# Performance work log

Measured on AMD Instinct MI355X. Metric: run time of the kernel, lower is better.

## Reference

```python
import jax, jax.numpy as jnp
import numpy as np

# dimensions (match init_kwargs / input_specs)
K = 25        # number of observation events
N_PER = 2048  # observations per event
B = 4096      # batch (sample_idx length)
D = 64        # input_dim
NDIM = 8      # memory_dim
H = D * NDIM  # hidden = 512
STEPS = 2     # euler ODE steps between consecutive obs_times
DT = 0.01
LOG_SQRT_2PI = 0.9189385332046727  # log(sqrt(2*pi))


def _xavier(key, shape):
    lim = np.sqrt(6.0 / (shape[0] + shape[1])).astype(np.float32)
    return jax.random.uniform(key, shape, jnp.float32, -lim, lim)


def setup_inputs() -> dict:
    key = jax.random.key(0)
    ks = jax.random.split(key, 10)
    # unique per-event indices (matches torch scatter-assign semantics)
    rng = np.random.RandomState(0)
    batch_idx = jnp.asarray(
        np.stack([rng.permutation(B)[:N_PER] for _ in range(K)]).reshape(-1),
        jnp.int32)
    return {
        "obs_times": jnp.arange(1, K + 1, dtype=jnp.float32) * (STEPS * DT),
        "event_pt": jnp.arange(K + 1, dtype=jnp.int32) * N_PER,
        "sample_idx": jnp.arange(B, dtype=jnp.int32),
        "X": jax.random.normal(ks[0], (K * N_PER, D), jnp.float32),
        "M": (jax.random.uniform(ks[1], (K * N_PER, D)) < 0.8).astype(jnp.float32),
        "batch_idx": batch_idx,
        # ODEFunc: Linear(H,H) -> Tanh -> Linear(H,H)
        "W_ode1": _xavier(ks[2], (H, H)), "b_ode1": jnp.zeros((H,), jnp.float32),
        "W_ode2": _xavier(ks[3], (H, H)), "b_ode2": jnp.zeros((H,), jnp.float32),
        # GRUCell(D, H)
        "W_ih": _xavier(ks[4], (3 * H, D)), "W_hh": _xavier(ks[5], (3 * H, H)),
        "b_ih": jnp.zeros((3 * H,), jnp.float32), "b_hh": jnp.zeros((3 * H,), jnp.float32),
        # p_model: Linear(H,H) -> ReLU -> (dropout=0) -> Linear(H, 2D)
        "Wp1": _xavier(ks[6], (H, H)), "bp1": jnp.zeros((H,), jnp.float32),
        "Wp2": _xavier(ks[7], (2 * D, H)), "bp2": jnp.zeros((2 * D,), jnp.float32),
    }


def reference(obs_times, event_pt, sample_idx, X, M, batch_idx,
              W_ode1, b_ode1, W_ode2, b_ode2,
              W_ih, W_hh, b_ih, b_hh, Wp1, bp1, Wp2, bp2):
    Xr = X.reshape(K, N_PER, D)
    Mr = M.reshape(K, N_PER, D)
    idx = batch_idx.reshape(K, N_PER)

    def ode_func(h):  # Linear -> Tanh -> Linear
        return jnp.tanh(h @ W_ode1.T + b_ode1) @ W_ode2.T + b_ode2

    def gru(x, h):  # torch GRUCell
        gi = x @ W_ih.T + b_ih
        gh = h @ W_hh.T + b_hh
        i_r, i_z, i_n = jnp.split(gi, 3, axis=1)
        h_r, h_z, h_n = jnp.split(gh, 3, axis=1)
        r = jax.nn.sigmoid(i_r + h_r)
        z = jax.nn.sigmoid(i_z + h_z)
        n = jnp.tanh(i_n + r * h_n)
        return (1.0 - z) * n + z * h

    def event_step(carry, inp):
        h, loss, m_tot = carry
        X_obs, M_obs, i_obs = inp
        # euler odeint over [0, dt], STEPS times to reach obs_time
        for _ in range(STEPS):
            h = h + DT * ode_func(h)
        # likelihood head on all samples, gather observed ones
        p = jax.nn.relu(h @ Wp1.T + bp1) @ Wp2.T + bp2       # [B, 2D]
        p_obs = p[i_obs]                                      # [N_PER, 2D]
        mean, logvar = jnp.split(p_obs, 2, axis=1)
        sigma = jnp.exp(0.5 * logvar)
        error = (X_obs - mean) / sigma
        losses = 0.5 * ((error * error + logvar + 2.0 * LOG_SQRT_2PI) * M_obs)
        # GRU update only on observed indices (scatter)
        h = h.at[i_obs].set(gru(X_obs, h[i_obs]))
        return (h, loss + losses.sum(), m_tot + M_obs.sum()), None

    h0 = jnp.zeros((B, H), jnp.float32)
    (h, loss, m_tot), _ = jax.lax.scan(event_step, (h0, jnp.float32(0.0), jnp.float32(0.0)), (Xr, Mr, idx))
    return (loss / m_tot, jnp.float32(0.0))
```

## Files before the change

kernel.cpp:

```cpp
#include <hip/hip_runtime.h>
#include <cstdint>
#include <cstddef>

#define BATCH 4096
#define DIM 64
#define HID 512
#define NPER 2048
#define KEV 25
#define DT_C 0.01f
#define LOG_SQRT_2PI_C 0.9189385332046727f

typedef __attribute__((ext_vector_type(8))) short short8;
typedef __attribute__((ext_vector_type(4))) float f32x4;

#define MFMA(a, b, c) __builtin_amdgcn_mfma_f32_16x16x32_bf16(a, b, c, 0, 0, 0)

__device__ __forceinline__ ushort f2bf(float f) {
    uint32_t u = __float_as_uint(f);
    u += 0x7FFF + ((u >> 16) & 1);
    return (ushort)(u >> 16);
}
__device__ __forceinline__ float sigmoidf_(float x) { return 1.0f / (1.0f + expf(-x)); }

__device__ __forceinline__ void gload_lds16(const ushort* g, ushort* l) {
    __builtin_amdgcn_global_load_lds(
        (const __attribute__((address_space(1))) void*)g,
        (__attribute__((address_space(3))) void*)l, 16, 0, 0);
}

__device__ __forceinline__ void wait_vm(int n) {
    if (n == 6)      asm volatile("s_waitcnt vmcnt(6)" ::: "memory");
    else if (n == 4) asm volatile("s_waitcnt vmcnt(4)" ::: "memory");
    else             asm volatile("s_waitcnt vmcnt(0)" ::: "memory");
}
#define BARRIER() __builtin_amdgcn_s_barrier()
#define SCHED0()  __builtin_amdgcn_sched_barrier(0)

__device__ __forceinline__ short8 frag64(const ushort* lds, int row, int ks, int lane) {
    int slot = ((ks << 2) + (lane >> 4)) ^ (row & 7);
    return *(const short8*)&lds[row * 64 + slot * 8];
}

template<int MODE>
__global__ __launch_bounds__(256) void ode_gemm(
    const ushort* __restrict__ A, const ushort* __restrict__ W,
    const float* __restrict__ bias, float* __restrict__ h, ushort* __restrict__ Cb)
{
    __shared__ __align__(16) ushort Alds[2][64 * 64];
    __shared__ __align__(16) ushort Blds[2][64 * 64];
    const int tid = threadIdx.x, lane = tid & 63, w = tid >> 6;
    const int wr = w >> 1, wc = w & 1;
    const int r0 = blockIdx.y * 64, c0 = blockIdx.x * 64;
    const int srow = lane >> 3;
    const int sg = ((lane & 7) ^ srow) << 3;
    const size_t ga0 = (size_t)(r0 + w * 16 + srow) * HID;
    const size_t ga1 = (size_t)(r0 + w * 16 + 8 + srow) * HID;
    const size_t gb0 = (size_t)(c0 + w * 16 + srow) * HID;
    const size_t gb1 = (size_t)(c0 + w * 16 + 8 + srow) * HID;

    f32x4 acc[2][2] = {};

    #define STAGE(b, k0) do {                                          \
        gload_lds16(A + ga0 + (k0) + sg, &Alds[b][(w * 16) * 64]);         \
        gload_lds16(A + ga1 + (k0) + sg, &Alds[b][(w * 16 + 8) * 64]);     \
        gload_lds16(W + gb0 + (k0) + sg, &Blds[b][(w * 16) * 64]);         \
        gload_lds16(W + gb1 + (k0) + sg, &Blds[b][(w * 16 + 8) * 64]);     \
    } while (0)

    STAGE(0, 0);
    STAGE(1, 64);
    #pragma unroll
    for (int t = 0; t < 8; ++t) {
        wait_vm((t < 7) ? 4 : 0);
        BARRIER();
        SCHED0();
        const ushort* Ab = &Alds[t & 1][0];
        const ushort* Bb = &Blds[t & 1][0];
        short8 af[2][2], bf[2][2];
        #pragma unroll
        for (int mi = 0; mi < 2; ++mi) {
            int r = wr * 32 + mi * 16 + (lane & 15);
            af[mi][0] = frag64(Ab, r, 0, lane);
            af[mi][1] = frag64(Ab, r, 1, lane);
        }
        #pragma unroll
        for (int ni = 0; ni < 2; ++ni) {
            int c = wc * 32 + ni * 16 + (lane & 15);
            bf[ni][0] = frag64(Bb, c, 0, lane);
            bf[ni][1] = frag64(Bb, c, 1, lane);
        }
        #pragma unroll
        for (int ks = 0; ks < 2; ++ks)
            #pragma unroll
            for (int mi = 0; mi < 2; ++mi)
                #pragma unroll
                for (int ni = 0; ni < 2; ++ni)
                    acc[mi][ni] = MFMA(af[mi][ks], bf[ni][ks], acc[mi][ni]);
        SCHED0();
        BARRIER();
        if (t + 2 < 8) STAGE(t & 1, (t + 2) * 64);
    }
    #undef STAGE

    #pragma unroll
    for (int mi = 0; mi < 2; ++mi)
        #pragma unroll
        for (int ni = 0; ni < 2; ++ni) {
            const int c = c0 + wc * 32 + ni * 16 + (lane & 15);
            const float bv = bias[c];
            #pragma unroll
            for (int ii = 0; ii < 4; ++ii) {
                const int r = r0 + wr * 32 + mi * 16 + ((lane >> 4) << 2) + ii;
                const size_t o = (size_t)r * HID + c;
                float v = acc[mi][ni][ii] + bv;
                if (MODE == 0) {
                    Cb[o] = f2bf(tanhf(v));
                } else {
                    float nh = h[o] + DT_C * v;
                    h[o] = nh; Cb[o] = f2bf(nh);
                }
            }
        }
}

template<int MODE>
__global__ __launch_bounds__(256) void event_gemm(
    const ushort* __restrict__ hb, const ushort* __restrict__ Xbk,
    const int* __restrict__ idx,
    const ushort* __restrict__ Bh, const ushort* __restrict__ Bx,
    const float* __restrict__ bias_i, const float* __restrict__ bias_h,
    float* __restrict__ rz, ushort* __restrict__ qb, float* __restrict__ h)
{
    __shared__ __align__(16) ushort Alds[2][64 * 64];
    __shared__ __align__(16) ushort Blds[2][64 * 64];
    const int tid = threadIdx.x, lane = tid & 63, w = tid >> 6;
    const int wr = w >> 1, wc = w & 1;
    const int r0t = blockIdx.y * 64;
    const int c0t = blockIdx.x * 64;
    const int NT = (MODE == 0) ? 8 : 9;

    const int srow = lane >> 3;
    const int sg = ((lane & 7) ^ srow) << 3;
    const int ar0 = r0t + w * 16 + srow, ar1 = r0t + w * 16 + 8 + srow;
    const size_t ga0 = (size_t)idx[ar0] * HID;
    const size_t ga1 = (size_t)idx[ar1] * HID;
    const size_t gb0 = (size_t)(c0t + w * 16 + srow) * HID;
    const size_t gb1 = (size_t)(c0t + w * 16 + 8 + srow) * HID;

    f32x4 acc[2][2] = {}, accX[2][2] = {};

    #define STAGE_P(b, p) do {                                                       \
        if ((p) < 8) {                                                               \
            gload_lds16(hb + ga0 + (p) * 64 + sg, &Alds[b][(w * 16) * 64]);              \
            gload_lds16(hb + ga1 + (p) * 64 + sg, &Alds[b][(w * 16 + 8) * 64]);          \
            gload_lds16(Bh + gb0 + (p) * 64 + sg, &Blds[b][(w * 16) * 64]);              \
            gload_lds16(Bh + gb1 + (p) * 64 + sg, &Blds[b][(w * 16 + 8) * 64]);          \
        } else {                                                                     \
            gload_lds16(Xbk + (size_t)ar0 * DIM + sg, &Alds[b][(w * 16) * 64]);          \
            gload_lds16(Xbk + (size_t)ar1 * DIM + sg, &Alds[b][(w * 16 + 8) * 64]);      \
            gload_lds16(Bx + (size_t)(c0t + w * 16 + srow) * DIM + sg,                   \
                        &Blds[b][(w * 16) * 64]);                                        \
            gload_lds16(Bx + (size_t)(c0t + w * 16 + 8 + srow) * DIM + sg,               \
                        &Blds[b][(w * 16 + 8) * 64]);                                    \
        }                                                                            \
    } while (0)

    STAGE_P(0, 0);
    STAGE_P(1, 1);
    #pragma unroll
    for (int t = 0; t < 9; ++t) {
        if (t >= NT) break;
        wait_vm((t + 1 < NT) ? 4 : 0);
        BARRIER();
        SCHED0();
        const ushort* Ab = &Alds[t & 1][0];
        const ushort* Bb = &Blds[t & 1][0];
        short8 af[2][2], bf[2][2];
        #pragma unroll
        for (int mi = 0; mi < 2; ++mi) {
            int r = wr * 32 + mi * 16 + (lane & 15);
            af[mi][0] = frag64(Ab, r, 0, lane);
            af[mi][1] = frag64(Ab, r, 1, lane);
        }
        #pragma unroll
        for (int ni = 0; ni < 2; ++ni) {
            int c = wc * 32 + ni * 16 + (lane & 15);
            bf[ni][0] = frag64(Bb, c, 0, lane);
            bf[ni][1] = frag64(Bb, c, 1, lane);
        }
        const bool toX = (MODE == 2) && (t == 8);
        #pragma unroll
        for (int ks = 0; ks < 2; ++ks)
            #pragma unroll
            for (int mi = 0; mi < 2; ++mi)
                #pragma unroll
                for (int ni = 0; ni < 2; ++ni) {
                    f32x4& a = toX ? accX[mi][ni] : acc[mi][ni];
                    a = MFMA(af[mi][ks], bf[ni][ks], a);
                }
        SCHED0();
        BARRIER();
        if (t + 2 < NT) STAGE_P(t & 1, t + 2);
    }
    #undef STAGE_P

    #pragma unroll
    for (int mi = 0; mi < 2; ++mi)
        #pragma unroll
        for (int ni = 0; ni < 2; ++ni) {
            const int c = c0t + wc * 32 + ni * 16 + (lane & 15);
            #pragma unroll
            for (int ii = 0; ii < 4; ++ii) {
                const int iobs = r0t + wr * 32 + mi * 16 + ((lane >> 4) << 2) + ii;
                float v = acc[mi][ni][ii];
                if (MODE == 0) {
                    qb[(size_t)iobs * HID + c] = f2bf(fmaxf(v + bias_h[c], 0.0f));
                } else if (MODE == 1) {
                    rz[(size_t)iobs * 1024 + c] = sigmoidf_(v + bias_i[c] + bias_h[c]);
                } else {
                    float vh = v + bias_h[c];
                    float vx = accX[mi][ni][ii] + bias_i[c];
                    float r = rz[(size_t)iobs * 1024 + c];
                    float z = rz[(size_t)iobs * 1024 + 512 + c];
                    float n = tanhf(vx + r * vh);
                    size_t o = (size_t)idx[iobs] * HID + c;
                    h[o] = (1.0f - z) * n + z * h[o];
                }
            }
        }
}

__global__ __launch_bounds__(256) void scatter_b16(
    const float* __restrict__ h, const int* __restrict__ idx, ushort* __restrict__ hb)
{
    int t = blockIdx.x * 256 + threadIdx.x;
    int i = t >> 6, j8 = (t & 63) << 3;
    size_t o = (size_t)idx[i] * HID + j8;
    float4 a = *(const float4*)&h[o];
    float4 b = *(const float4*)&h[o + 4];
    ushort ob[8] = {f2bf(a.x), f2bf(a.y), f2bf(a.z), f2bf(a.w),
                    f2bf(b.x), f2bf(b.y), f2bf(b.z), f2bf(b.w)};
    *(ushort4*)&hb[o]     = *(ushort4*)&ob[0];
    *(ushort4*)&hb[o + 4] = *(ushort4*)&ob[4];
}

__device__ __forceinline__ void block_atomic_sum(float v, float* acc) {
    __shared__ float red[4];
    #pragma unroll
    for (int off = 32; off > 0; off >>= 1) v += __shfl_down(v, off);
    int lane = threadIdx.x & 63, wid = threadIdx.x >> 6;
    if (lane == 0) red[wid] = v;
    __syncthreads();
    if (threadIdx.x == 0) atomicAdd(acc, red[0] + red[1] + red[2] + red[3]);
}

__global__ __launch_bounds__(256) void p_loss(
    const ushort* __restrict__ qb, const ushort* __restrict__ Wp2b,
    const float* __restrict__ bp2, const float* __restrict__ Xk,
    const float* __restrict__ Mk, float* __restrict__ loss_acc)
{
    __shared__ __align__(16) ushort Alds[2][64 * 64];
    __shared__ __align__(16) ushort Blds[2][128 * 64];
    __shared__ float Plds[64 * 128];
    const int tid = threadIdx.x, lane = tid & 63, w = tid >> 6;
    const int wr = w >> 1, wc = w & 1;
    const int r0t = blockIdx.x * 64;
    const int arow = w * 16 + (lane >> 3);
    const int sg = ((lane & 7) ^ ((lane >> 3) & 7)) << 3;

    #define STAGE_PL(b, k0) do {                                                        \
        gload_lds16(qb + (size_t)(r0t + arow) * HID + (k0) + sg, &Alds[b][(w * 16) * 64]);  \
        gload_lds16(qb + (size_t)(r0t + arow + 8) * HID + (k0) + sg,                        \
                    &Alds[b][(w * 16 + 8) * 64]);                                           \
        _Pragma("unroll")                                                                   \
        for (int j_ = 0; j_ < 4; ++j_) {                                                    \
            int g_ = w * 4 + j_;                                                            \
            int rw_ = g_ * 8 + (lane >> 3);                                                 \
            gload_lds16(Wp2b + (size_t)rw_ * HID + (k0) + (((lane & 7) ^ (rw_ & 7)) << 3),  \
                        &Blds[b][g_ * 8 * 64]);                                             \
        }                                                                               \
    } while (0)

    f32x4 acc[2][4] = {};
    STAGE_PL(0, 0);
    STAGE_PL(1, 64);
    #pragma unroll
    for (int t = 0; t < 8; ++t) {
        wait_vm((t < 7) ? 6 : 0);
        BARRIER();
        SCHED0();
        const ushort* Ab = &Alds[t & 1][0];
        const ushort* Bb = &Blds[t & 1][0];
        short8 af[2][2], bf[4][2];
        #pragma unroll
        for (int mi = 0; mi < 2; ++mi) {
            int r = wr * 32 + mi * 16 + (lane & 15);
            af[mi][0] = frag64(Ab, r, 0, lane);
            af[mi][1] = frag64(Ab, r, 1, lane);
        }
        #pragma unroll
        for (int ni = 0; ni < 4; ++ni) {
            int c = wc * 64 + ni * 16 + (lane & 15);
            bf[ni][0] = frag64(Bb, c, 0, lane);
            bf[ni][1] = frag64(Bb, c, 1, lane);
        }
        #pragma unroll
        for (int ks = 0; ks < 2; ++ks)
            #pragma unroll
            for (int mi = 0; mi < 2; ++mi)
                #pragma unroll
                for (int ni = 0; ni < 4; ++ni)
                    acc[mi][ni] = MFMA(af[mi][ks], bf[ni][ks], acc[mi][ni]);
        SCHED0();
        BARRIER();
        if (t + 2 < 8) STAGE_PL(t & 1, (t + 2) * 64);
    }
    #undef STAGE_PL

    #pragma unroll
    for (int mi = 0; mi < 2; ++mi)
        #pragma unroll
        for (int ni = 0; ni < 4; ++ni) {
            int c = wc * 64 + ni * 16 + (lane & 15);
            float bv = bp2[c];
            #pragma unroll
            for (int ii = 0; ii < 4; ++ii) {
                int r = wr * 32 + mi * 16 + ((lane >> 4) << 2) + ii;
                Plds[r * 128 + c] = acc[mi][ni][ii] + bv;
            }
        }
    __syncthreads();

    float local = 0.0f;
    for (int t = tid; t < 64 * 64; t += 256) {
        int r = t >> 6, jj = t & 63;
        float mean = Plds[r * 128 + jj];
        float lv   = Plds[r * 128 + 64 + jj];
        int g = r0t + r;
        float err = (Xk[g * 64 + jj] - mean) * expf(-0.5f * lv);
        local += 0.5f * (err * err + lv + 2.0f * LOG_SQRT_2PI_C) * Mk[g * 64 + jj];
    }
    block_atomic_sum(local, loss_acc);
}

__global__ __launch_bounds__(256) void f2b4_kernel(
    const float* __restrict__ s, ushort* __restrict__ d, int n4)
{
    int t = blockIdx.x * 256 + threadIdx.x;
    if (t >= n4) return;
    float4 v = ((const float4*)s)[t];
    ushort4 o; o.x = f2bf(v.x); o.y = f2bf(v.y); o.z = f2bf(v.z); o.w = f2bf(v.w);
    ((ushort4*)d)[t] = o;
}

__global__ __launch_bounds__(256) void msum_kernel(
    const float* __restrict__ M, int n, float* __restrict__ m_acc)
{
    float v = 0.0f;
    for (int t = blockIdx.x * 256 + threadIdx.x; t < n; t += gridDim.x * 256)
        v += M[t];
    block_atomic_sum(v, m_acc);
}

__global__ void finalize_kernel(const float* __restrict__ sums, float* __restrict__ out) {
    if (threadIdx.x == 0) { out[0] = sums[0] / sums[1]; out[1] = 0.0f; }
}

extern "C" void kernel_launch(void* const* d_in, const int* in_sizes, int n_in,
                              void* d_out, int out_size, void* d_ws, size_t ws_size,
                              hipStream_t stream) {
    const float* X      = (const float*)d_in[3];
    const float* M      = (const float*)d_in[4];
    const int* batch_idx= (const int*)  d_in[5];
    const float* W_ode1 = (const float*)d_in[6];
    const float* b_ode1 = (const float*)d_in[7];
    const float* W_ode2 = (const float*)d_in[8];
    const float* b_ode2 = (const float*)d_in[9];
    const float* W_ih   = (const float*)d_in[10];
    const float* W_hh   = (const float*)d_in[11];
    const float* b_ih   = (const float*)d_in[12];
    const float* b_hh   = (const float*)d_in[13];
    const float* Wp1    = (const float*)d_in[14];
    const float* bp1    = (const float*)d_in[15];
    const float* Wp2    = (const float*)d_in[16];
    const float* bp2    = (const float*)d_in[17];
    float* out = (float*)d_out;

    float* ws   = (float*)d_ws;
    float* h    = ws;
    float* rz   = h  + (size_t)BATCH * HID;
    float* sums = rz + (size_t)NPER * 1024;
    ushort* hb   = (ushort*)(sums + 16);
    ushort* tbb  = hb   + (size_t)BATCH * HID;
    ushort* qb   = tbb  + (size_t)BATCH * HID;
    ushort* Xb   = qb   + (size_t)NPER * HID;
    ushort* W1b  = Xb   + (size_t)KEV * NPER * DIM;
    ushort* W2b  = W1b  + (size_t)HID * HID;
    ushort* Wp1b = W2b  + (size_t)HID * HID;
    ushort* Wp2b = Wp1b + (size_t)HID * HID;
    ushort* Wihb = Wp2b + (size_t)2 * DIM * HID;
    ushort* Whhb = Wihb + (size_t)(3 * HID) * DIM;

    hipMemsetAsync(h,    0, (size_t)BATCH * HID * sizeof(float), stream);
    hipMemsetAsync(hb,   0, (size_t)BATCH * HID * sizeof(ushort), stream);
    hipMemsetAsync(sums, 0, 2 * sizeof(float), stream);

    dim3 blk(256);
    auto cvt = [&](const float* s, ushort* d, size_t n) {
        f2b4_kernel<<<dim3((unsigned)((n / 4 + 255) / 256)), blk, 0, stream>>>(s, d, (int)(n / 4));
    };
    cvt(W_ode1, W1b,  (size_t)HID * HID);
    cvt(W_ode2, W2b,  (size_t)HID * HID);
    cvt(Wp1,    Wp1b, (size_t)HID * HID);
    cvt(Wp2,    Wp2b, (size_t)2 * DIM * HID);
    cvt(W_ih,   Wihb, (size_t)3 * HID * DIM);
    cvt(W_hh,   Whhb, (size_t)3 * HID * HID);
    cvt(X,      Xb,   (size_t)KEV * NPER * DIM);

    msum_kernel<<<1024, blk, 0, stream>>>(M, KEV * NPER * DIM, sums + 1);

    dim3 gOde(HID / 64, BATCH / 64);

    for (int k = 0; k < KEV; ++k) {
        const float*  Xk  = X  + (size_t)k * NPER * DIM;
        const float*  Mk  = M  + (size_t)k * NPER * DIM;
        const ushort* Xbk = Xb + (size_t)k * NPER * DIM;
        const int*   idxk = batch_idx + (size_t)k * NPER;

        for (int s = 0; s < 2; ++s) {
            ode_gemm<0><<<gOde, blk, 0, stream>>>(hb,  W1b, b_ode1, nullptr, tbb);
            ode_gemm<1><<<gOde, blk, 0, stream>>>(tbb, W2b, b_ode2, h,       hb);
        }

        event_gemm<0><<<dim3(8, 32), blk, 0, stream>>>(
            hb, nullptr, idxk, Wp1b, nullptr, nullptr, bp1, nullptr, qb, nullptr);
        p_loss<<<32, blk, 0, stream>>>(qb, Wp2b, bp2, Xk, Mk, sums);

        event_gemm<1><<<dim3(16, 32), blk, 0, stream>>>(
            hb, Xbk, idxk, Whhb, Wihb, b_ih, b_hh, rz, nullptr, nullptr);
        event_gemm<2><<<dim3(8, 32), blk, 0, stream>>>(
            hb, Xbk, idxk, Whhb + (size_t)1024 * HID, Wihb + (size_t)1024 * DIM,
            b_ih + 1024, b_hh + 1024, rz, nullptr, h);
        scatter_b16<<<NPER * HID / 8 / 256, blk, 0, stream>>>(h, idxk, hb);
    }

    finalize_kernel<<<1, 64, 0, stream>>>(sums, out);
}
```

Baseline: 2.381 ms.

## Replace per-event kernel launches with one persistent cooperative kernel using grid syncs

Fuses the whole 25-event loop (ODE GEMMs, likelihood head, GRU gate GEMMs, scatter update) into a single cooperative kernel of 256 blocks of 512 threads, with grid.sync between dependent stages. The aim is to remove the roughly 200 kernel launches and their tail/launch gaps. It also reorganises the GRU epilogue: the n-gate GEMM now writes separate hidden and input partials, and the gate combine happens in the scatter stage. p_loss and the GRU scatter run concurrently on different blocks. The old multi-kernel path is kept as a fallback if the cooperative launch fails. Grid-wide barriers and a fixed 256-block grid may limit occupancy and add sync cost.

Result: slower. 6.597 ms (+177.1%).

```diff
diff --git a/kernel.cpp b/kernel.cpp
--- a/kernel.cpp
+++ b/kernel.cpp
@@ -1,12 +1,17 @@
 #include <hip/hip_runtime.h>
+#include <hip/hip_cooperative_groups.h>
 #include <cstdint>
 #include <cstddef>
+
+namespace cg = cooperative_groups;
 
 #define BATCH 4096
 #define DIM 64
 #define HID 512
 #define NPER 2048
 #define KEV 25
+#define NBLK 256
+#define NTHR 512
 #define DT_C 0.01f
 #define LOG_SQRT_2PI_C 0.9189385332046727f
 
@@ -14,6 +19,8 @@
 typedef __attribute__((ext_vector_type(4))) float f32x4;
 
 #define MFMA(a, b, c) __builtin_amdgcn_mfma_f32_16x16x32_bf16(a, b, c, 0, 0, 0)
+#define BARRIER() __builtin_amdgcn_s_barrier()
+#define SCHED0()  __builtin_amdgcn_sched_barrier(0)
 
 __device__ __forceinline__ ushort f2bf(float f) {
     uint32_t u = __float_as_uint(f);
@@ -27,22 +34,338 @@
         (const __attribute__((address_space(1))) void*)g,
         (__attribute__((address_space(3))) void*)l, 16, 0, 0);
 }
-
 __device__ __forceinline__ void wait_vm(int n) {
-    if (n == 6)      asm volatile("s_waitcnt vmcnt(6)" ::: "memory");
+    if (n == 3)      asm volatile("s_waitcnt vmcnt(3)" ::: "memory");
     else if (n == 4) asm volatile("s_waitcnt vmcnt(4)" ::: "memory");
+    else if (n == 6) asm volatile("s_waitcnt vmcnt(6)" ::: "memory");
     else             asm volatile("s_waitcnt vmcnt(0)" ::: "memory");
 }
-#define BARRIER() __builtin_amdgcn_s_barrier()
-#define SCHED0()  __builtin_amdgcn_sched_barrier(0)
 
 __device__ __forceinline__ short8 frag64(const ushort* lds, int row, int ks, int lane) {
     int slot = ((ks << 2) + (lane >> 4)) ^ (row & 7);
     return *(const short8*)&lds[row * 64 + slot * 8];
 }
 
+
+__device__ __forceinline__ void gemm128(
+    ushort* smem, int w, int lane,
+    const ushort* gA0, const ushort* gA1, const ushort* gB0,
+    const ushort* tA0, const ushort* tA1, const ushort* tB0,
+    int NT, bool tailToX, f32x4 acc[2][2], f32x4 accX[2][2])
+{
+    const int wr = w >> 1, wc = w & 1;
+    auto stage = [&](int b, int p) {
+        ushort* A = smem + b * 8192;
+        ushort* B = smem + 16384 + b * 4096;
+        if (p < 8) {
+            gload_lds16(gA0 + (size_t)p * 64, &A[(w * 16) * 64]);
+            gload_lds16(gA1 + (size_t)p * 64, &A[(w * 16 + 8) * 64]);
+            gload_lds16(gB0 + (size_t)p * 64, &B[(w * 8) * 64]);
+        } else {
+            gload_lds16(tA0, &A[(w * 16) * 64]);
+            gload_lds16(tA1, &A[(w * 16 + 8) * 64]);
+            gload_lds16(tB0, &B[(w * 8) * 64]);
+        }
+    };
+    stage(0, 0);
+    stage(1, 1);
+    for (int t = 0; t < NT; ++t) {
+        wait_vm((t + 1 < NT) ? 3 : 0);
+        BARRIER();
+        SCHED0();
+        const ushort* Ab = smem + (t & 1) * 8192;
+        const ushort* Bb = smem + 16384 + (t & 1) * 4096;
+        short8 af[2][2], bf[2][2];
+        #pragma unroll
+        for (int mi = 0; mi < 2; ++mi) {
+            int r = wr * 32 + mi * 16 + (lane & 15);
+            af[mi][0] = frag64(Ab, r, 0, lane);
+            af[mi][1] = frag64(Ab, r, 1, lane);
+        }
+        #pragma unroll
+        for (int ni = 0; ni < 2; ++ni) {
+            int c = wc * 32 + ni * 16 + (lane & 15);
+            bf[ni][0] = frag64(Bb, c, 0, lane);
+            bf[ni][1] = frag64(Bb, c, 1, lane);
+        }
+        const bool toX = tailToX && (t == 8);
+        #pragma unroll
+        for (int ks = 0; ks < 2; ++ks)
+            #pragma unroll
+            for (int mi = 0; mi < 2; ++mi)
+                #pragma unroll
+                for (int ni = 0; ni < 2; ++ni) {
+                    f32x4& a = toX ? accX[mi][ni] : acc[mi][ni];
+                    a = MFMA(af[mi][ks], bf[ni][ks], a);
+                }
+        SCHED0();
+        BARRIER();
+        if (t + 2 < NT) stage(t & 1, t + 2);
+    }
+}
+
+__device__ void p_loss_task(
+    ushort* smem, int task, const ushort* qb, const ushort* Wp2,
+    const float* bp2, const float* Xk, const float* Mk, float* sums,
+    int tid, int lane, int w)
+{
+    const int wr = w >> 1, wc = w & 1;
+    const int r0t = task * 128;
+    const int srow = lane >> 3;
+    const int sg = ((lane & 7) ^ srow) << 3;
+
+    auto stage = [&](int b, int k0) {
+        ushort* A = smem + b * 8192;
+        ushort* B = smem + 16384 + b * 8192;
+        gload_lds16(qb + (size_t)(r0t + w * 16 + srow) * HID + k0 + sg, &A[(w * 16) * 64]);
+        gload_lds16(qb + (size_t)(r0t + w * 16 + 8 + srow) * HID + k0 + sg, &A[(w * 16 + 8) * 64]);
+        gload_lds16(Wp2 + (size_t)(w * 16 + srow) * HID + k0 + sg, &B[(w * 16) * 64]);
+        gload_lds16(Wp2 + (size_t)(w * 16 + 8 + srow) * HID + k0 + sg, &B[(w * 16 + 8) * 64]);
+    };
+    f32x4 acc[2][4] = {};
+    stage(0, 0);
+    stage(1, 64);
+    for (int t = 0; t < 8; ++t) {
+        wait_vm((t < 7) ? 4 : 0);
+        BARRIER();
+        SCHED0();
+        const ushort* Ab = smem + (t & 1) * 8192;
+        const ushort* Bb = smem + 16384 + (t & 1) * 8192;
+        short8 af[2][2], bf[4][2];
+        #pragma unroll
+        for (int mi = 0; mi < 2; ++mi) {
+            int r = wr * 32 + mi * 16 + (lane & 15);
+            af[mi][0] = frag64(Ab, r, 0, lane);
+            af[mi][1] = frag64(Ab, r, 1, lane);
+        }
+        #pragma unroll
+        for (int ni = 0; ni < 4; ++ni) {
+            int c = wc * 64 + ni * 16 + (lane & 15);
+            bf[ni][0] = frag64(Bb, c, 0, lane);
+            bf[ni][1] = frag64(Bb, c, 1, lane);
+        }
+        #pragma unroll
+        for (int ks = 0; ks < 2; ++ks)
+            #pragma unroll
+            for (int mi = 0; mi < 2; ++mi)
+                #pragma unroll
+                for (int ni = 0; ni < 4; ++ni)
+                    acc[mi][ni] = MFMA(af[mi][ks], bf[ni][ks], acc[mi][ni]);
+        SCHED0();
+        BARRIER();
+        if (t + 2 < 8) stage(t & 1, (t + 2) * 64);
+    }
+
+    float* Plds = (float*)smem;
+    #pragma unroll
+    for (int mi = 0; mi < 2; ++mi)
+        #pragma unroll
+        for (int ni = 0; ni < 4; ++ni) {
+            int c = wc * 64 + ni * 16 + (lane & 15);
+            float bv = bp2[c];
+            #pragma unroll
+            for (int ii = 0; ii < 4; ++ii) {
+                int r = wr * 32 + mi * 16 + ((lane >> 4) << 2) + ii;
+                Plds[r * 128 + c] = acc[mi][ni][ii] + bv;
+            }
+        }
+    __syncthreads();
+
+    float local = 0.0f;
+    for (int t = tid; t < 128 * 64; t += NTHR) {
+        int r = t >> 6, jj = t & 63;
+        float mean = Plds[r * 128 + jj];
+        float lv   = Plds[r * 128 + 64 + jj];
+        int g = r0t + r;
+        float err = (Xk[(size_t)g * 64 + jj] - mean) * expf(-0.5f * lv);
+        local += 0.5f * (err * err + lv + 2.0f * LOG_SQRT_2PI_C) * Mk[(size_t)g * 64 + jj];
+    }
+    #pragma unroll
+    for (int o = 32; o > 0; o >>= 1) local += __shfl_down(local, o);
+    if (lane == 0) atomicAdd(sums, local);
+    __syncthreads();
+}
+
+__global__ __launch_bounds__(NTHR, 2) void persist(
+    const float* __restrict__ Xf, const float* __restrict__ Mf,
+    const int* __restrict__ bidx, const ushort* __restrict__ Xb,
+    const ushort* __restrict__ W1, const ushort* __restrict__ W2,
+    const ushort* __restrict__ Wp1, const ushort* __restrict__ Wp2,
+    const ushort* __restrict__ Wih, const ushort* __restrict__ Whh,
+    const float* __restrict__ b1, const float* __restrict__ b2,
+    const float* __restrict__ bih, const float* __restrict__ bhh,
+    const float* __restrict__ bp1, const float* __restrict__ bp2,
+    float* __restrict__ h, ushort* __restrict__ hb, ushort* __restrict__ tbb,
+    ushort* __restrict__ qb, float* __restrict__ rz,
+    float* __restrict__ nh_, float* __restrict__ nx_,
+    float* __restrict__ sums, float* __restrict__ out)
+{
+    __shared__ __align__(16) ushort smem[32768];
+    cg::grid_group grid = cg::this_grid();
+    const int tid = threadIdx.x, lane = tid & 63, w = tid >> 6;
+    const int wr = w >> 1, wc = w & 1;
+    const int bid = blockIdx.x;
+    const int srow = lane >> 3;
+    const int sg = ((lane & 7) ^ srow) << 3;
+
+    {
+        float v = 0.0f;
+        const float4* M4 = (const float4*)Mf;
+        const int n4 = KEV * NPER * DIM / 4;
+        for (int t = bid * NTHR + tid; t < n4; t += NBLK * NTHR) {
+            float4 x = M4[t]; v += x.x + x.y + x.z + x.w;
+        }
+        #pragma unroll
+        for (int o = 32; o > 0; o >>= 1) v += __shfl_down(v, o);
+        if (lane == 0) atomicAdd(sums + 1, v);
+    }
+
+    f32x4 accX[2][2];
+
+    for (int k = 0; k < KEV; ++k) {
+        const ushort* Xbk = Xb + (size_t)k * NPER * DIM;
+        const int* idxk = bidx + (size_t)k * NPER;
+        const float* Xk = Xf + (size_t)k * NPER * DIM;
+        const float* Mk = Mf + (size_t)k * NPER * DIM;
+
+        const int r0 = (bid >> 3) * 128, c0 = (bid & 7) * 64;
+        for (int s = 0; s < 2; ++s) {
+            {
+                f32x4 acc[2][2] = {};
+                gemm128(smem, w, lane,
+                    hb + (size_t)(r0 + w * 16 + srow) * HID + sg,
+                    hb + (size_t)(r0 + w * 16 + 8 + srow) * HID + sg,
+                    W1 + (size_t)(c0 + w * 8 + srow) * HID + sg,
+                    nullptr, nullptr, nullptr, 8, false, acc, accX);
+                #pragma unroll
+                for (int mi = 0; mi < 2; ++mi)
+                    #pragma unroll
+                    for (int ni = 0; ni < 2; ++ni) {
+                        const int c = c0 + wc * 32 + ni * 16 + (lane & 15);
+                        const float bv = b1[c];
+                        #pragma unroll
+                        for (int ii = 0; ii < 4; ++ii) {
+                            const int r = r0 + wr * 32 + mi * 16 + ((lane >> 4) << 2) + ii;
+                            tbb[(size_t)r * HID + c] = f2bf(tanhf(acc[mi][ni][ii] + bv));
+                        }
+                    }
+            }
+            grid.sync();
+            {
+                f32x4 acc[2][2] = {};
+                gemm128(smem, w, lane,
+                    tbb + (size_t)(r0 + w * 16 + srow) * HID + sg,
+                    tbb + (size_t)(r0 + w * 16 + 8 + srow) * HID + sg,
+                    W2 + (size_t)(c0 + w * 8 + srow) * HID + sg,
+                    nullptr, nullptr, nullptr, 8, false, acc, accX);
+                #pragma unroll
+                for (int mi = 0; mi < 2; ++mi)
+                    #pragma unroll
+                    for (int ni = 0; ni < 2; ++ni) {
+                        const int c = c0 + wc * 32 + ni * 16 + (lane & 15);
+                        const float bv = b2[c];
+                        #pragma unroll
+                        for (int ii = 0; ii < 4; ++ii) {
+                            const int r = r0 + wr * 32 + mi * 16 + ((lane >> 4) << 2) + ii;
+                            const size_t o = (size_t)r * HID + c;
+                            float nh = h[o] + DT_C * (acc[mi][ni][ii] + bv);
+                            h[o] = nh; hb[o] = f2bf(nh);
+                        }
+                    }
+            }
+            grid.sync();
+        }
+
+        for (int rd = 0; rd < 2; ++rd) {
+            const int task = bid + rd * NBLK;
+            int mode, r0t, c0t;
+            const ushort *Bh, *Bx = Xbk;
+            bool tailX = false;
+            if (task < 128) {
+                mode = 0; r0t = (task >> 3) * 128; c0t = (task & 7) * 64; Bh = Wp1;
+            } else if (task < 384) {
+                int t2 = task - 128;
+                mode = 1; r0t = (t2 >> 4) * 128; c0t = (t2 & 15) * 64;
+                Bh = Whh; Bx = Wih;
+            } else {
+                int t3 = task - 384;
+                mode = 2; r0t = (t3 >> 3) * 128; c0t = (t3 & 7) * 64;
+                Bh = Whh + (size_t)1024 * HID; Bx = Wih + (size_t)1024 * DIM; tailX = true;
+            }
+            const int ar0 = r0t + w * 16 + srow, ar1 = r0t + w * 16 + 8 + srow;
+            const int NT = (mode == 0) ? 8 : 9;
+
+            f32x4 acc[2][2] = {};
+            #pragma unroll
+            for (int mi = 0; mi < 2; ++mi)
+                #pragma unroll
+                for (int ni = 0; ni < 2; ++ni) accX[mi][ni] = (f32x4){0.f, 0.f, 0.f, 0.f};
+            gemm128(smem, w, lane,
+                hb + (size_t)idxk[ar0] * HID + sg,
+                hb + (size_t)idxk[ar1] * HID + sg,
+                Bh + (size_t)(c0t + w * 8 + srow) * HID + sg,
+                Xbk + (size_t)ar0 * DIM + sg,
+                Xbk + (size_t)ar1 * DIM + sg,
+                (mode == 0) ? (Xbk + sg) : (Bx + (size_t)(c0t + w * 8 + srow) * DIM + sg),
+                NT, tailX, acc, accX);
+
+            #pragma unroll
+            for (int mi = 0; mi < 2; ++mi)
+                #pragma unroll
+                for (int ni = 0; ni < 2; ++ni) {
+                    const int c = c0t + wc * 32 + ni * 16 + (lane & 15);
+                    #pragma unroll
+                    for (int ii = 0; ii < 4; ++ii) {
+                        const int iobs = r0t + wr * 32 + mi * 16 + ((lane >> 4) << 2) + ii;
+                        float v = acc[mi][ni][ii];
+                        if (mode == 0) {
+                            qb[(size_t)iobs * HID + c] = f2bf(fmaxf(v + bp1[c], 0.0f));
+                        } else if (mode == 1) {
+                            rz[(size_t)iobs * 1024 + c] = sigmoidf_(v + bih[c] + bhh[c]);
+                        } else {
+                            nh_[(size_t)iobs * HID + c] = v + bhh[1024 + c];
+                            nx_[(size_t)iobs * HID + c] = accX[mi][ni][ii] + bih[1024 + c];
+                        }
+                    }
+                }
+        }
+        grid.sync();
+
+        if (bid < 16) {
+            p_loss_task(smem, bid, qb, Wp2, bp2, Xk, Mk, sums, tid, lane, w);
+        } else if (bid < 144) {
+            const int tt = bid - 16;
+            #pragma unroll
+            for (int i = 0; i < 4; ++i) {
+                int v = tt * 2048 + tid + i * NTHR;
+                int row = v >> 7, j4 = (v & 127) << 2;
+                float4 rr = *(const float4*)&rz[(size_t)row * 1024 + j4];
+                float4 zz = *(const float4*)&rz[(size_t)row * 1024 + 512 + j4];
+                float4 hn = *(const float4*)&nh_[(size_t)row * HID + j4];
+                float4 xn = *(const float4*)&nx_[(size_t)row * HID + j4];
+                size_t o = (size_t)idxk[row] * HID + j4;
+                float4 hv = *(const float4*)&h[o];
+                float4 res; ushort4 ob;
+                #define C1(c) { float n = tanhf(xn.c + rr.c * hn.c); \
+                                res.c = (1.0f - zz.c) * n + zz.c * hv.c; ob.c = f2bf(res.c); }
+                C1(x) C1(y) C1(z) C1(w)
+                #undef C1
+                *(float4*)&h[o] = res;
+                *(ushort4*)&hb[o] = ob;
+            }
+        }
+        grid.sync();
+    }
+
+    if (bid == 0 && tid == 0) { out[0] = sums[0] / sums[1]; out[1] = 0.0f; }
+}
+
+__device__ __forceinline__ short8 frag64b(const ushort* lds, int row, int ks, int lane) {
+    return frag64(lds, row, ks, lane);
+}
+
 template<int MODE>
-__global__ __launch_bounds__(256) void ode_gemm(
+__global__ __launch_bounds__(256) void fb_ode_gemm(
     const ushort* __restrict__ A, const ushort* __restrict__ W,
     const float* __restrict__ bias, float* __restrict__ h, ushort* __restrict__ Cb)
 {
@@ -57,37 +380,29 @@
     const size_t ga1 = (size_t)(r0 + w * 16 + 8 + srow) * HID;
     const size_t gb0 = (size_t)(c0 + w * 16 + srow) * HID;
     const size_t gb1 = (size_t)(c0 + w * 16 + 8 + srow) * HID;
-
     f32x4 acc[2][2] = {};
-
-    #define STAGE(b, k0) do {                                          \
-        gload_lds16(A + ga0 + (k0) + sg, &Alds[b][(w * 16) * 64]);         \
-        gload_lds16(A + ga1 + (k0) + sg, &Alds[b][(w * 16 + 8) * 64]);     \
-        gload_lds16(W + gb0 + (k0) + sg, &Blds[b][(w * 16) * 64]);         \
-        gload_lds16(W + gb1 + (k0) + sg, &Blds[b][(w * 16 + 8) * 64]);     \
-    } while (0)
-
-    STAGE(0, 0);
-    STAGE(1, 64);
+    #define STG(b, k0) do { \
+        gload_lds16(A + ga0 + (k0) + sg, &Alds[b][(w * 16) * 64]); \
+        gload_lds16(A + ga1 + (k0) + sg, &Alds[b][(w * 16 + 8) * 64]); \
+        gload_lds16(W + gb0 + (k0) + sg, &Blds[b][(w * 16) * 64]); \
+        gload_lds16(W + gb1 + (k0) + sg, &Blds[b][(w * 16 + 8) * 64]); } while (0)
+    STG(0, 0); STG(1, 64);
     #pragma unroll
     for (int t = 0; t < 8; ++t) {
         wait_vm((t < 7) ? 4 : 0);
-        BARRIER();
-        SCHED0();
+        BARRIER(); SCHED0();
         const ushort* Ab = &Alds[t & 1][0];
         const ushort* Bb = &Blds[t & 1][0];
         short8 af[2][2], bf[2][2];
         #pragma unroll
         for (int mi = 0; mi < 2; ++mi) {
             int r = wr * 32 + mi * 16 + (lane & 15);
-            af[mi][0] = frag64(Ab, r, 0, lane);
-            af[mi][1] = frag64(Ab, r, 1, lane);
+            af[mi][0] = frag64b(Ab, r, 0, lane); af[mi][1] = frag64b(Ab, r, 1, lane);
         }
         #pragma unroll
         for (int ni = 0; ni < 2; ++ni) {
             int c = wc * 32 + ni * 16 + (lane & 15);
-            bf[ni][0] = frag64(Bb, c, 0, lane);
-            bf[ni][1] = frag64(Bb, c, 1, lane);
+            bf[ni][0] = frag64b(Bb, c, 0, lane); bf[ni][1] = frag64b(Bb, c, 1, lane);
         }
         #pragma unroll
         for (int ks = 0; ks < 2; ++ks)
@@ -96,12 +411,10 @@
                 #pragma unroll
                 for (int ni = 0; ni < 2; ++ni)
                     acc[mi][ni] = MFMA(af[mi][ks], bf[ni][ks], acc[mi][ni]);
-        SCHED0();
-        BARRIER();
-        if (t + 2 < 8) STAGE(t & 1, (t + 2) * 64);
-    }
-    #undef STAGE
-
+        SCHED0(); BARRIER();
+        if (t + 2 < 8) STG(t & 1, (t + 2) * 64);
+    }
+    #undef STG
     #pragma unroll
     for (int mi = 0; mi < 2; ++mi)
         #pragma unroll
@@ -113,18 +426,14 @@
                 const int r = r0 + wr * 32 + mi * 16 + ((lane >> 4) << 2) + ii;
                 const size_t o = (size_t)r * HID + c;
                 float v = acc[mi][ni][ii] + bv;
-                if (MODE == 0) {
-                    Cb[o] = f2bf(tanhf(v));
-                } else {
-                    float nh = h[o] + DT_C * v;
-                    h[o] = nh; Cb[o] = f2bf(nh);
-                }
+                if (MODE == 0) Cb[o] = f2bf(tanhf(v));
+                else { float nh = h[o] + DT_C * v; h[o] = nh; Cb[o] = f2bf(nh); }
             }
         }
 }
 
 template<int MODE>
-__global__ __launch_bounds__(256) void event_gemm(
+__global__ __launch_bounds__(256) void fb_event_gemm(
     const ushort* __restrict__ hb, const ushort* __restrict__ Xbk,
     const int* __restrict__ idx,
     const ushort* __restrict__ Bh, const ushort* __restrict__ Bx,
@@ -138,7 +447,6 @@
     const int r0t = blockIdx.y * 64;
     const int c0t = blockIdx.x * 64;
     const int NT = (MODE == 0) ? 8 : 9;
-
     const int srow = lane >> 3;
     const int sg = ((lane & 7) ^ srow) << 3;
     const int ar0 = r0t + w * 16 + srow, ar1 = r0t + w * 16 + 8 + srow;
@@ -146,47 +454,37 @@
     const size_t ga1 = (size_t)idx[ar1] * HID;
     const size_t gb0 = (size_t)(c0t + w * 16 + srow) * HID;
     const size_t gb1 = (size_t)(c0t + w * 16 + 8 + srow) * HID;
-
     f32x4 acc[2][2] = {}, accX[2][2] = {};
-
-    #define STAGE_P(b, p) do {                                                       \
-        if ((p) < 8) {                                                               \
-            gload_lds16(hb + ga0 + (p) * 64 + sg, &Alds[b][(w * 16) * 64]);              \
-            gload_lds16(hb + ga1 + (p) * 64 + sg, &Alds[b][(w * 16 + 8) * 64]);          \
-            gload_lds16(Bh + gb0 + (p) * 64 + sg, &Blds[b][(w * 16) * 64]);              \
-            gload_lds16(Bh + gb1 + (p) * 64 + sg, &Blds[b][(w * 16 + 8) * 64]);          \
-        } else {                                                                     \
-            gload_lds16(Xbk + (size_t)ar0 * DIM + sg, &Alds[b][(w * 16) * 64]);          \
-            gload_lds16(Xbk + (size_t)ar1 * DIM + sg, &Alds[b][(w * 16 + 8) * 64]);      \
-            gload_lds16(Bx + (size_t)(c0t + w * 16 + srow) * DIM + sg,                   \
-                        &Blds[b][(w * 16) * 64]);                                        \
-            gload_lds16(Bx + (size_t)(c0t + w * 16 + 8 + srow) * DIM + sg,               \
-                        &Blds[b][(w * 16 + 8) * 64]);                                    \
-        }                                                                            \
-    } while (0)
-
-    STAGE_P(0, 0);
-    STAGE_P(1, 1);
+    #define STGP(b, p) do { \
+        if ((p) < 8) { \
+            gload_lds16(hb + ga0 + (p) * 64 + sg, &Alds[b][(w * 16) * 64]); \
+            gload_lds16(hb + ga1 + (p) * 64 + sg, &Alds[b][(w * 16 + 8) * 64]); \
+            gload_lds16(Bh + gb0 + (p) * 64 + sg, &Blds[b][(w * 16) * 64]); \
+            gload_lds16(Bh + gb1 + (p) * 64 + sg, &Blds[b][(w * 16 + 8) * 64]); \
+        } else { \
+            gload_lds16(Xbk + (size_t)ar0 * DIM + sg, &Alds[b][(w * 16) * 64]); \
+            gload_lds16(Xbk + (size_t)ar1 * DIM + sg, &Alds[b][(w * 16 + 8) * 64]); \
+            gload_lds16(Bx + (size_t)(c0t + w * 16 + srow) * DIM + sg, &Blds[b][(w * 16) * 64]); \
+            gload_lds16(Bx + (size_t)(c0t + w * 16 + 8 + srow) * DIM + sg, &Blds[b][(w * 16 + 8) * 64]); \
+        } } while (0)
+    STGP(0, 0); STGP(1, 1);
     #pragma unroll
     for (int t = 0; t < 9; ++t) {
         if (t >= NT) break;
         wait_vm((t + 1 < NT) ? 4 : 0);
-        BARRIER();
-        SCHED0();
+        BARRIER(); SCHED0();
         const ushort* Ab = &Alds[t & 1][0];
         const ushort* Bb = &Blds[t & 1][0];
         short8 af[2][2], bf[2][2];
         #pragma unroll
         for (int mi = 0; mi < 2; ++mi) {
             int r = wr * 32 + mi * 16 + (lane & 15);
-            af[mi][0] = frag64(Ab, r, 0, lane);
-            af[mi][1] = frag64(Ab, r, 1, lane);
+            af[mi][0] = frag64b(Ab, r, 0, lane); af[mi][1] = frag64b(Ab, r, 1, lane);
         }
         #pragma unroll
         for (int ni = 0; ni < 2; ++ni) {
             int c = wc * 32 + ni * 16 + (lane & 15);
-            bf[ni][0] = frag64(Bb, c, 0, lane);
-            bf[ni][1] = frag64(Bb, c, 1, lane);
+            bf[ni][0] = frag64b(Bb, c, 0, lane); bf[ni][1] = frag64b(Bb, c, 1, lane);
         }
         const bool toX = (MODE == 2) && (t == 8);
         #pragma unroll
@@ -198,12 +496,10 @@
                     f32x4& a = toX ? accX[mi][ni] : acc[mi][ni];
                     a = MFMA(af[mi][ks], bf[ni][ks], a);
                 }
-        SCHED0();
-        BARRIER();
-        if (t + 2 < NT) STAGE_P(t & 1, t + 2);
-    }
-    #undef STAGE_P
-
+        SCHED0(); BARRIER();
+        if (t + 2 < NT) STGP(t & 1, t + 2);
+    }
+    #undef STGP
     #pragma unroll
     for (int mi = 0; mi < 2; ++mi)
         #pragma unroll
@@ -230,7 +526,7 @@
         }
 }
 
-__global__ __launch_bounds__(256) void scatter_b16(
+__global__ __launch_bounds__(256) void fb_scatter_b16(
     const float* __restrict__ h, const int* __restrict__ idx, ushort* __restrict__ hb)
 {
     int t = blockIdx.x * 256 + threadIdx.x;
@@ -254,55 +550,42 @@
     if (threadIdx.x == 0) atomicAdd(acc, red[0] + red[1] + red[2] + red[3]);
 }
 
-__global__ __launch_bounds__(256) void p_loss(
+__global__ __launch_bounds__(256) void fb_p_loss(
     const ushort* __restrict__ qb, const ushort* __restrict__ Wp2b,
     const float* __restrict__ bp2, const float* __restrict__ Xk,
     const float* __restrict__ Mk, float* __restrict__ loss_acc)
 {
-    __shared__ __align__(16) ushort Alds[2][64 * 64];
-    __shared__ __align__(16) ushort Blds[2][128 * 64];
+    __shared__ __align__(16) ushort Alds[64 * 64];
+    __shared__ __align__(16) ushort Blds[128 * 64];
     __shared__ float Plds[64 * 128];
     const int tid = threadIdx.x, lane = tid & 63, w = tid >> 6;
     const int wr = w >> 1, wc = w & 1;
     const int r0t = blockIdx.x * 64;
     const int arow = w * 16 + (lane >> 3);
     const int sg = ((lane & 7) ^ ((lane >> 3) & 7)) << 3;
-
-    #define STAGE_PL(b, k0) do {                                                        \
-        gload_lds16(qb + (size_t)(r0t + arow) * HID + (k0) + sg, &Alds[b][(w * 16) * 64]);  \
-        gload_lds16(qb + (size_t)(r0t + arow + 8) * HID + (k0) + sg,                        \
-                    &Alds[b][(w * 16 + 8) * 64]);                                           \
-        _Pragma("unroll")                                                                   \
-        for (int j_ = 0; j_ < 4; ++j_) {                                                    \
-            int g_ = w * 4 + j_;                                                            \
-            int rw_ = g_ * 8 + (lane >> 3);                                                 \
-            gload_lds16(Wp2b + (size_t)rw_ * HID + (k0) + (((lane & 7) ^ (rw_ & 7)) << 3),  \
-                        &Blds[b][g_ * 8 * 64]);                                             \
-        }                                                                               \
-    } while (0)
-
     f32x4 acc[2][4] = {};
-    STAGE_PL(0, 0);
-    STAGE_PL(1, 64);
-    #pragma unroll
-    for (int t = 0; t < 8; ++t) {
-        wait_vm((t < 7) ? 6 : 0);
-        BARRIER();
-        SCHED0();
-        const ushort* Ab = &Alds[t & 1][0];
-        const ushort* Bb = &Blds[t & 1][0];
+    for (int k0 = 0; k0 < HID; k0 += 64) {
+        __syncthreads();
+        gload_lds16(qb + (size_t)(r0t + arow) * HID + k0 + sg, &Alds[(w * 16) * 64]);
+        gload_lds16(qb + (size_t)(r0t + arow + 8) * HID + k0 + sg, &Alds[(w * 16 + 8) * 64]);
+        #pragma unroll
+        for (int j = 0; j < 4; ++j) {
+            int g = w * 4 + j;
+            int rw = g * 8 + (lane >> 3);
+            gload_lds16(Wp2b + (size_t)rw * HID + k0 + (((lane & 7) ^ (rw & 7)) << 3),
+                        &Blds[g * 8 * 64]);
+        }
+        __syncthreads();
         short8 af[2][2], bf[4][2];
         #pragma unroll
         for (int mi = 0; mi < 2; ++mi) {
             int r = wr * 32 + mi * 16 + (lane & 15);
-            af[mi][0] = frag64(Ab, r, 0, lane);
-            af[mi][1] = frag64(Ab, r, 1, lane);
+            af[mi][0] = frag64b(Alds, r, 0, lane); af[mi][1] = frag64b(Alds, r, 1, lane);
         }
         #pragma unroll
         for (int ni = 0; ni < 4; ++ni) {
             int c = wc * 64 + ni * 16 + (lane & 15);
-            bf[ni][0] = frag64(Bb, c, 0, lane);
-            bf[ni][1] = frag64(Bb, c, 1, lane);
+            bf[ni][0] = frag64b(Blds, c, 0, lane); bf[ni][1] = frag64b(Blds, c, 1, lane);
         }
         #pragma unroll
         for (int ks = 0; ks < 2; ++ks)
@@ -311,12 +594,7 @@
                 #pragma unroll
                 for (int ni = 0; ni < 4; ++ni)
                     acc[mi][ni] = MFMA(af[mi][ks], bf[ni][ks], acc[mi][ni]);
-        SCHED0();
-        BARRIER();
-        if (t + 2 < 8) STAGE_PL(t & 1, (t + 2) * 64);
-    }
-    #undef STAGE_PL
-
+    }
     #pragma unroll
     for (int mi = 0; mi < 2; ++mi)
         #pragma unroll
@@ -330,7 +608,6 @@
             }
         }
     __syncthreads();
-
     float local = 0.0f;
     for (int t = tid; t < 64 * 64; t += 256) {
         int r = t >> 6, jj = t & 63;
@@ -386,20 +663,22 @@
     const float* bp2    = (const float*)d_in[17];
     float* out = (float*)d_out;
 
-    float* ws   = (float*)d_ws;
-    float* h    = ws;
-    float* rz   = h  + (size_t)BATCH * HID;
-    float* sums = rz + (size_t)NPER * 1024;
+    float* ws    = (float*)d_ws;
+    float* h     = ws;
+    float* rz    = h   + (size_t)BATCH * HID;
+    float* nh_   = rz  + (size_t)NPER * 1024;
+    float* nx_   = nh_ + (size_t)NPER * HID;
+    float* sums  = nx_ + (size_t)NPER * HID;
     ushort* hb   = (ushort*)(sums + 16);
-    ushort* tbb  = hb   + (size_t)BATCH * HID;
-    ushort* qb   = tbb  + (size_t)BATCH * HID;
-    ushort* Xb   = qb   + (size_t)NPER * HID;
-    ushort* W1b  = Xb   + (size_t)KEV * NPER * DIM;
-    ushort* W2b  = W1b  + (size_t)HID * HID;
-    ushort* Wp1b = W2b  + (size_t)HID * HID;
+    ushort* tbb  = hb  + (size_t)BATCH * HID;
+    ushort* qb   = tbb + (size_t)BATCH * HID;
+    ushort* Xb   = qb  + (size_t)NPER * HID;
+    ushort* W1b  = Xb  + (size_t)KEV * NPER * DIM;
+    ushort* W2b  = W1b + (size_t)HID * HID;
+    ushort* Wp1b = W2b + (size_t)HID * HID;
     ushort* Wp2b = Wp1b + (size_t)HID * HID;
     ushort* Wihb = Wp2b + (size_t)2 * DIM * HID;
-    ushort* Whhb = Wihb + (size_t)(3 * HID) * DIM;
+    ushort* Whhb = Wihb + (size_t)3 * HID * DIM;
 
     hipMemsetAsync(h,    0, (size_t)BATCH * HID * sizeof(float), stream);
     hipMemsetAsync(hb,   0, (size_t)BATCH * HID * sizeof(ushort), stream);
@@ -417,32 +696,50 @@
     cvt(W_hh,   Whhb, (size_t)3 * HID * HID);
     cvt(X,      Xb,   (size_t)KEV * NPER * DIM);
 
+    const float* Xf = X; const float* Mf = M; const int* bidx = batch_idx;
+    const ushort* Xb_c = Xb; const ushort* W1_c = W1b; const ushort* W2_c = W2b;
+    const ushort* Wp1_c = Wp1b; const ushort* Wp2_c = Wp2b;
+    const ushort* Wih_c = Wihb; const ushort* Whh_c = Whhb;
+    const float* b1_c = b_ode1; const float* b2_c = b_ode2;
+    const float* bih_c = b_ih; const float* bhh_c = b_hh;
+    const float* bp1_c = bp1; const float* bp2_c = bp2;
+    float* h_c = h; ushort* hb_c = hb; ushort* tbb_c = tbb; ushort* qb_c = qb;
+    float* rz_c = rz; float* nh_c = nh_; float* nx_c = nx_;
+    float* sums_c = sums; float* out_c = out;
+
+    void* kargs[] = {
+        (void*)&Xf, (void*)&Mf, (void*)&bidx, (void*)&Xb_c,
+        (void*)&W1_c, (void*)&W2_c, (void*)&Wp1_c, (void*)&Wp2_c,
+        (void*)&Wih_c, (void*)&Whh_c,
+        (void*)&b1_c, (void*)&b2_c, (void*)&bih_c, (void*)&bhh_c,
+        (void*)&bp1_c, (void*)&bp2_c,
+        (void*)&h_c, (void*)&hb_c, (void*)&tbb_c, (void*)&qb_c,
+        (void*)&rz_c, (void*)&nh_c, (void*)&nx_c, (void*)&sums_c, (void*)&out_c
+    };
+    hipError_t cerr = hipLaunchCooperativeKernel((const void*)persist, dim3(NBLK), dim3(NTHR),
+                                                 kargs, 0, stream);
+    if (cerr == hipSuccess) return;
+
     msum_kernel<<<1024, blk, 0, stream>>>(M, KEV * NPER * DIM, sums + 1);
-
     dim3 gOde(HID / 64, BATCH / 64);
-
     for (int k = 0; k < KEV; ++k) {
         const float*  Xk  = X  + (size_t)k * NPER * DIM;
         const float*  Mk  = M  + (size_t)k * NPER * DIM;
         const ushort* Xbk = Xb + (size_t)k * NPER * DIM;
         const int*   idxk = batch_idx + (size_t)k * NPER;
-
         for (int s = 0; s < 2; ++s) {
-            ode_gemm<0><<<gOde, blk, 0, stream>>>(hb,  W1b, b_ode1, nullptr, tbb);
-            ode_gemm<1><<<gOde, blk, 0, stream>>>(tbb, W2b, b_ode2, h,       hb);
-        }
-
-        event_gemm<0><<<dim3(8, 32), blk, 0, stream>>>(
+            fb_ode_gemm<0><<<gOde, blk, 0, stream>>>(hb,  W1b, b_ode1, nullptr, tbb);
+            fb_ode_gemm<1><<<gOde, blk, 0, stream>>>(tbb, W2b, b_ode2, h,       hb);
+        }
+        fb_event_gemm<0><<<dim3(8, 32), blk, 0, stream>>>(
             hb, nullptr, idxk, Wp1b, nullptr, nullptr, bp1, nullptr, qb, nullptr);
-        p_loss<<<32, blk, 0, stream>>>(qb, Wp2b, bp2, Xk, Mk, sums);
-
-        event_gemm<1><<<dim3(16, 32), blk, 0, stream>>>(
+        fb_p_loss<<<32, blk, 0, stream>>>(qb, Wp2b, bp2, Xk, Mk, sums);
+        fb_event_gemm<1><<<dim3(16, 32), blk, 0, stream>>>(
             hb, Xbk, idxk, Whhb, Wihb, b_ih, b_hh, rz, nullptr, nullptr);
-        event_gemm<2><<<dim3(8, 32), blk, 0, stream>>>(
+        fb_event_gemm<2><<<dim3(8, 32), blk, 0, stream>>>(
             hb, Xbk, idxk, Whhb + (size_t)1024 * HID, Wihb + (size_t)1024 * DIM,
             b_ih + 1024, b_hh + 1024, rz, nullptr, h);
-        scatter_b16<<<NPER * HID / 8 / 256, blk, 0, stream>>>(h, idxk, hb);
-    }
-
+        fb_scatter_b16<<<NPER * HID / 8 / 256, blk, 0, stream>>>(h, idxk, hb);
+    }
     finalize_kernel<<<1, 64, 0, stream>>>(sums, out);
 }
```
